# Kernel optimization log

Hardware: AMD Instinct MI355X
Metric: run time of the kernel (lower is better)

The kernel has to match this reference:

```python
import jax, jax.numpy as jnp
import numpy as np

BS, N, DIM, HEADS = 4, 2048, 512, 8
HEAD_DIM = DIM // HEADS
SCALE = HEAD_DIM ** 0.5
NEG = -1000000.0


def setup_inputs() -> dict:
    key = jax.random.key(0)
    ks = jax.random.split(key, 6)
    x = jax.random.normal(ks[0], (BS, N, DIM), dtype=jnp.float32)
    mask = jax.random.randint(ks[1], (BS, N), 0, 2, dtype=jnp.int32)
    s = 1.0 / np.sqrt(DIM)
    Wq = jax.random.normal(ks[2], (DIM, DIM), dtype=jnp.float32) * s
    Wk = jax.random.normal(ks[3], (DIM, DIM), dtype=jnp.float32) * s
    Wv = jax.random.normal(ks[4], (DIM, DIM), dtype=jnp.float32) * s
    Wo = jax.random.normal(ks[5], (DIM, DIM), dtype=jnp.float32) * s
    return {"x": x, "Wq": Wq, "Wk": Wk, "Wv": Wv, "Wo": Wo, "mask": mask}


def reference(x, Wq, Wk, Wv, Wo, mask):
    # q,k,v: (bs, n, dim) -> (bs, h, n, d)
    def split_heads(t):
        return t.reshape(BS, N, HEADS, HEAD_DIM).transpose(0, 2, 1, 3)
    q = split_heads(x @ Wq.T)
    k = split_heads(x @ Wk.T)
    v = split_heads(x @ Wv.T)
    # scores: (bs, h, n, n)
    scores = jnp.einsum('bhqd,bhkd->bhqk', q, k) / SCALE
    # key-padding mask broadcast over heads and query positions
    keep = (mask == 1)[:, None, None, :]  # (bs,1,1,n)
    scores = jnp.where(keep, scores, NEG)
    attn = jax.nn.softmax(scores, axis=-1)
    out = jnp.einsum('bhqk,bhkd->bhqd', attn, v)
    out = out.transpose(0, 2, 1, 3).reshape(BS, N, DIM)
    return out @ Wo.T
```

## Files before the change

### kernel.cpp

```cpp
#include <hip/hip_runtime.h>
#include <hip/hip_bf16.h>

#define BS 4
#define SEQ 2048
#define DIM 512
#define HEADS 8
#define HD 64
#define ROWS (BS*SEQ)
#define SCL2E 0.1803368801111244f
#define NEGB (-1.4426950408889634e6f)

typedef __attribute__((ext_vector_type(8))) short bf16x8;
typedef __attribute__((ext_vector_type(4))) short bf16x4;
typedef __attribute__((ext_vector_type(4))) float floatx4;
typedef unsigned short u16;
typedef unsigned int u32;

__device__ __forceinline__ u16 f2bf(float f) {
    union { float f; unsigned u; } v; v.f = f;
    unsigned r = v.u + 0x7fff + ((v.u >> 16) & 1);
    return (u16)(r >> 16);
}

__device__ __forceinline__ unsigned pack2bf(float a, float b) {
#if __has_builtin(__builtin_amdgcn_cvt_pk_bf16_f32)
    typedef __attribute__((ext_vector_type(2))) __bf16 bf2;
    union { bf2 v; unsigned u; } cv;
    cv.v = __builtin_amdgcn_cvt_pk_bf16_f32(a, b);
    return cv.u;
#else
    return (unsigned)f2bf(a) | ((unsigned)f2bf(b) << 16);
#endif
}

__device__ __forceinline__ float fexp2(float x) {
#if __has_builtin(__builtin_amdgcn_exp2f)
    return __builtin_amdgcn_exp2f(x);
#else
    return __expf(x * 0.6931471805599453f);
#endif
}

__device__ __forceinline__ void gload16(const u16* g, u16* l) {
    __builtin_amdgcn_global_load_lds(
        (const __attribute__((address_space(1))) u32*)g,
        (__attribute__((address_space(3))) u32*)l, 16, 0, 0);
}

__global__ __launch_bounds__(256) void convert_all(
    const float* __restrict__ x, const float* __restrict__ Wq,
    const float* __restrict__ Wk, const float* __restrict__ Wv,
    const float* __restrict__ Wo, const int* __restrict__ mask,
    u16* __restrict__ xb, u16* __restrict__ wqb,
    u16* __restrict__ wkb, u16* __restrict__ wvb,
    u16* __restrict__ wob, float* __restrict__ biasf)
{
    int i = blockIdx.x * 256 + threadIdx.x;
    if (i < 1048576 + 262144) {
        const float* src; u16* dst; int off;
        if (i < 1048576) { src = x; dst = xb; off = i; }
        else {
            int j = i - 1048576; int seg = j >> 16; off = j & 65535;
            src = seg == 0 ? Wq : seg == 1 ? Wk : seg == 2 ? Wv : Wo;
            dst = seg == 0 ? wqb : seg == 1 ? wkb : seg == 2 ? wvb : wob;
        }
        float4 v = ((const float4*)src)[off];
        ushort4 o;
        o.x = f2bf(v.x); o.y = f2bf(v.y); o.z = f2bf(v.z); o.w = f2bf(v.w);
        ((ushort4*)dst)[off] = o;
    } else {
        int jb = i - 1310720;
        int4 mv = ((const int4*)mask)[jb];
        float4 bo;
        bo.x = (mv.x == 1) ? 0.f : NEGB;
        bo.y = (mv.y == 1) ? 0.f : NEGB;
        bo.z = (mv.z == 1) ? 0.f : NEGB;
        bo.w = (mv.w == 1) ? 0.f : NEGB;
        ((float4*)biasf)[jb] = bo;
    }
}

__global__ __launch_bounds__(256, 3) void gemm_qkv_fused(
    const u16* __restrict__ A, const u16* __restrict__ Wcat,
    u16* __restrict__ Oq, u16* __restrict__ Okf, u16* __restrict__ Ovf)
{
    __shared__ u16 ldsA[8192];
    __shared__ u16 ldsB[8192];

    int n0 = blockIdx.x * 128;
    int m0 = blockIdx.y * 128;
    int tid = threadIdx.x;
    int w = tid >> 6, lane = tid & 63, quad = lane >> 4, l16 = lane & 15;
    int mo = (w & 1) * 64, no = (w >> 1) * 64;
    int l7 = l16 & 7;

    int sr = lane >> 3, sc = lane & 7, gc = sc ^ sr;
    const u16* gA0 = A    + (long)(m0 + sr) * DIM + gc * 8;
    const u16* gB0 = Wcat + (long)(n0 + sr) * DIM + gc * 8;

    floatx4 acc[4][4];
    #pragma unroll
    for (int mt = 0; mt < 4; mt++)
        #pragma unroll
        for (int nt = 0; nt < 4; nt++) acc[mt][nt] = (floatx4){0.f,0.f,0.f,0.f};

    for (int k0 = 0; k0 < DIM; k0 += 64) {
        #pragma unroll
        for (int i = 0; i < 4; i++) {
            int ch = w * 4 + i;
            gload16(gA0 + (long)ch * 8 * DIM + k0, &ldsA[ch * 512]);
            gload16(gB0 + (long)ch * 8 * DIM + k0, &ldsB[ch * 512]);
        }
        __syncthreads();

        #pragma unroll
        for (int kc = 0; kc < 2; kc++) {
            int swz = ((kc * 4 + quad) ^ l7) * 8;
            bf16x8 af[4], bf[4];
            #pragma unroll
            for (int t4 = 0; t4 < 4; t4++) {
                af[t4] = *(const bf16x8*)&ldsA[(mo + t4*16 + l16) * 64 + swz];
                bf[t4] = *(const bf16x8*)&ldsB[(no + t4*16 + l16) * 64 + swz];
            }
            #pragma unroll
            for (int mt = 0; mt < 4; mt++)
                #pragma unroll
                for (int nt = 0; nt < 4; nt++)
                    acc[mt][nt] = __builtin_amdgcn_mfma_f32_16x16x32_bf16(
                        af[mt], bf[nt], acc[mt][nt], 0, 0, 0);
        }
        __syncthreads();
    }

    int seg = n0 >> 9;
    if (seg == 0) {
        #pragma unroll
        for (int mt = 0; mt < 4; mt++)
            #pragma unroll
            for (int nt = 0; nt < 4; nt++)
                #pragma unroll
                for (int r = 0; r < 4; r++) {
                    int row = m0 + mo + mt*16 + quad*4 + r;
                    int col9 = (n0 + no + nt*16 + l16) & 511;
                    int b = row >> 11, n = row & 2047, h = col9 >> 6, d = col9 & 63;
                    Oq[(((long)(b * HEADS + h) * SEQ + n) << 6) + d] = f2bf(acc[mt][nt][r]);
                }
    } else if (seg == 1) {
        #pragma unroll
        for (int mt = 0; mt < 4; mt++)
            #pragma unroll
            for (int nt = 0; nt < 4; nt++)
                #pragma unroll
                for (int r = 0; r < 4; r++) {
                    int row = m0 + mo + mt*16 + quad*4 + r;
                    int col9 = (n0 + no + nt*16 + l16) & 511;
                    int b = row >> 11, keyn = row & 2047, h = col9 >> 6, dd = col9 & 63;
                    int kt = keyn >> 6, ntk = (keyn >> 4) & 3, l16k = keyn & 15;
                    int g = dd >> 5, quadk = (dd >> 3) & 3, j = dd & 7;
                    long offv = ((long)((b*HEADS + h)*32 + kt) << 12)
                              + ((ntk*2 + g) << 9) + ((quadk*16 + l16k) << 3) + j;
                    Okf[offv] = f2bf(acc[mt][nt][r] * SCL2E);
                }
    } else {
        #pragma unroll
        for (int mt = 0; mt < 4; mt++)
            #pragma unroll
            for (int nt = 0; nt < 4; nt++) {
                int rowb = m0 + mo + mt*16 + quad*4;
                int col9 = (n0 + no + nt*16 + l16) & 511;
                int b = rowb >> 11, keyn = rowb & 2047, h = col9 >> 6;
                int tile = (keyn >> 6) & 31;
                long offv = ((long)((b*HEADS + h)*32 + tile) << 12)
                          + ((long)(mt >> 1) << 11) + (nt << 9)
                          + ((quad*16 + l16) << 3) + ((mt & 1) << 2);
                ushort4 st;
                st.x = f2bf(acc[mt][nt][0]); st.y = f2bf(acc[mt][nt][1]);
                st.z = f2bf(acc[mt][nt][2]); st.w = f2bf(acc[mt][nt][3]);
                *(ushort4*)&Ovf[offv] = st;
            }
    }
}

__global__ __launch_bounds__(256, 3) void flash_attn(
    const u16* __restrict__ Q, const u16* __restrict__ Kf,
    const u16* __restrict__ Vf, const float* __restrict__ biasf,
    u16* __restrict__ ctx)
{
    __shared__ float red[4224];

    int bx = blockIdx.x;
    int cx = bx & 7, sx = bx >> 3;
    int gg = ((sx >> 5) << 3) | cx;
    int qi = sx & 31;
    int q0 = qi * 64;
    int h  = gg & 7;
    int b  = gg >> 3;
    int bh = b * HEADS + h;

    int tid = threadIdx.x;
    int w = tid >> 6, lane = tid & 63, quad = lane >> 4, l16 = lane & 15;
    int wq = w >> 1, wk = w & 1;

    bf16x8 qA0, qA1, qB0, qB1;
    {
        const u16* qp = Q + ((long)bh * SEQ + q0 + wq*32 + l16) * HD + quad * 8;
        qA0 = *(const bf16x8*)(qp);
        qA1 = *(const bf16x8*)(qp + 32);
        qB0 = *(const bf16x8*)(qp + 16*HD);
        qB1 = *(const bf16x8*)(qp + 16*HD + 32);
    }

    const u16* Kw = Kf + ((long)bh << 17) + wk*2048 + lane*8;
    const u16* Vw = Vf + ((long)bh << 17) + wk*2048 + lane*8;
    const float* bw = biasf + b * SEQ + wk*32 + quad*4;

    short one_s = (l16 == 0) ? (short)0x3F80 : (short)0;
    bf16x8 ones8 = { one_s, one_s, one_s, one_s, one_s, one_s, one_s, one_s };

    bf16x8 kA0 = *(const bf16x8*)(Kw);
    bf16x8 kA1 = *(const bf16x8*)(Kw + 512);
    bf16x8 kB0 = *(const bf16x8*)(Kw + 1024);
    bf16x8 kB1 = *(const bf16x8*)(Kw + 1536);
    bf16x8 vb0 = *(const bf16x8*)(Vw);
    bf16x8 vb1 = *(const bf16x8*)(Vw + 512);
    bf16x8 vb2 = *(const bf16x8*)(Vw + 1024);
    bf16x8 vb3 = *(const bf16x8*)(Vw + 1536);
    float4 bv0 = *(const float4*)(bw);
    float4 bv1 = *(const float4*)(bw + 16);

    floatx4 oA[4], oB[4], o5A, o5B;
    #pragma unroll
    for (int ct = 0; ct < 4; ct++) {
        oA[ct] = (floatx4){0.f,0.f,0.f,0.f};
        oB[ct] = (floatx4){0.f,0.f,0.f,0.f};
    }
    o5A = (floatx4){0.f,0.f,0.f,0.f};
    o5B = (floatx4){0.f,0.f,0.f,0.f};

    #pragma unroll 2
    for (int it = 0; it < 32; it++) {
        bf16x8 kA0n=kA0, kA1n=kA1, kB0n=kB0, kB1n=kB1;
        bf16x8 vb0n=vb0, vb1n=vb1, vb2n=vb2, vb3n=vb3;
        float4 bv0n=bv0, bv1n=bv1;
        if (it < 31) {
            const u16* kp = Kw + (long)(it+1)*4096;
            const u16* vp = Vw + (long)(it+1)*4096;
            kA0n = *(const bf16x8*)(kp);
            kA1n = *(const bf16x8*)(kp + 512);
            kB0n = *(const bf16x8*)(kp + 1024);
            kB1n = *(const bf16x8*)(kp + 1536);
            vb0n = *(const bf16x8*)(vp);
            vb1n = *(const bf16x8*)(vp + 512);
            vb2n = *(const bf16x8*)(vp + 1024);
            vb3n = *(const bf16x8*)(vp + 1536);
            bv0n = *(const float4*)(bw + (it+1)*64);
            bv1n = *(const float4*)(bw + (it+1)*64 + 16);
        }

        {
            floatx4 s0, s1;
            s0[0] = bv0.x; s0[1] = bv0.y; s0[2] = bv0.z; s0[3] = bv0.w;
            s1[0] = bv1.x; s1[1] = bv1.y; s1[2] = bv1.z; s1[3] = bv1.w;
            s0 = __builtin_amdgcn_mfma_f32_16x16x32_bf16(kA0, qA0, s0, 0, 0, 0);
            s0 = __builtin_amdgcn_mfma_f32_16x16x32_bf16(kA1, qA1, s0, 0, 0, 0);
            s1 = __builtin_amdgcn_mfma_f32_16x16x32_bf16(kB0, qA0, s1, 0, 0, 0);
            s1 = __builtin_amdgcn_mfma_f32_16x16x32_bf16(kB1, qA1, s1, 0, 0, 0);
            float p0 = fexp2(s0[0]);
            float p1 = fexp2(s0[1]);
            float p2 = fexp2(s0[2]);
            float p3 = fexp2(s0[3]);
            float p4 = fexp2(s1[0]);
            float p5 = fexp2(s1[1]);
            float p6 = fexp2(s1[2]);
            float p7 = fexp2(s1[3]);
            union { bf16x8 v; unsigned u[4]; } pu;
            pu.u[0] = pack2bf(p0, p1);
            pu.u[1] = pack2bf(p2, p3);
            pu.u[2] = pack2bf(p4, p5);
            pu.u[3] = pack2bf(p6, p7);
            oA[0] = __builtin_amdgcn_mfma_f32_16x16x32_bf16(pu.v, vb0, oA[0], 0, 0, 0);
            oA[1] = __builtin_amdgcn_mfma_f32_16x16x32_bf16(pu.v, vb1, oA[1], 0, 0, 0);
            oA[2] = __builtin_amdgcn_mfma_f32_16x16x32_bf16(pu.v, vb2, oA[2], 0, 0, 0);
            oA[3] = __builtin_amdgcn_mfma_f32_16x16x32_bf16(pu.v, vb3, oA[3], 0, 0, 0);
            o5A  = __builtin_amdgcn_mfma_f32_16x16x32_bf16(pu.v, ones8, o5A, 0, 0, 0);
        }
        {
            floatx4 s0, s1;
            s0[0] = bv0.x; s0[1] = bv0.y; s0[2] = bv0.z; s0[3] = bv0.w;
            s1[0] = bv1.x; s1[1] = bv1.y; s1[2] = bv1.z; s1[3] = bv1.w;
            s0 = __builtin_amdgcn_mfma_f32_16x16x32_bf16(kA0, qB0, s0, 0, 0, 0);
            s0 = __builtin_amdgcn_mfma_f32_16x16x32_bf16(kA1, qB1, s0, 0, 0, 0);
            s1 = __builtin_amdgcn_mfma_f32_16x16x32_bf16(kB0, qB0, s1, 0, 0, 0);
            s1 = __builtin_amdgcn_mfma_f32_16x16x32_bf16(kB1, qB1, s1, 0, 0, 0);
            float p0 = fexp2(s0[0]);
            float p1 = fexp2(s0[1]);
            float p2 = fexp2(s0[2]);
            float p3 = fexp2(s0[3]);
            float p4 = fexp2(s1[0]);
            float p5 = fexp2(s1[1]);
            float p6 = fexp2(s1[2]);
            float p7 = fexp2(s1[3]);
            union { bf16x8 v; unsigned u[4]; } pu;
            pu.u[0] = pack2bf(p0, p1);
            pu.u[1] = pack2bf(p2, p3);
            pu.u[2] = pack2bf(p4, p5);
            pu.u[3] = pack2bf(p6, p7);
            oB[0] = __builtin_amdgcn_mfma_f32_16x16x32_bf16(pu.v, vb0, oB[0], 0, 0, 0);
            oB[1] = __builtin_amdgcn_mfma_f32_16x16x32_bf16(pu.v, vb1, oB[1], 0, 0, 0);
            oB[2] = __builtin_amdgcn_mfma_f32_16x16x32_bf16(pu.v, vb2, oB[2], 0, 0, 0);
            oB[3] = __builtin_amdgcn_mfma_f32_16x16x32_bf16(pu.v, vb3, oB[3], 0, 0, 0);
            o5B  = __builtin_amdgcn_mfma_f32_16x16x32_bf16(pu.v, ones8, o5B, 0, 0, 0);
        }

        kA0 = kA0n; kA1 = kA1n; kB0 = kB0n; kB1 = kB1n;
        vb0 = vb0n; vb1 = vb1n; vb2 = vb2n; vb3 = vb3n;
        bv0 = bv0n; bv1 = bv1n;
    }

    floatx4* ldsv = (floatx4*)red;
    float* ldsf = red;
    int Town = wq*2 + wk;
    int Tpar = wq*2 + (wk ^ 1);

    if (wk == 0) {
        #pragma unroll
        for (int ct = 0; ct < 4; ct++)
            ldsv[Tpar*256 + ct*64 + lane] = oB[ct];
    } else {
        #pragma unroll
        for (int ct = 0; ct < 4; ct++)
            ldsv[Tpar*256 + ct*64 + lane] = oA[ct];
    }
    if (l16 == 0) {
        #pragma unroll
        for (int r = 0; r < 4; r++) {
            ldsf[4096 + ((wq*2 + 0)*2 + wk)*16 + quad*4 + r] = o5A[r];
            ldsf[4096 + ((wq*2 + 1)*2 + wk)*16 + quad*4 + r] = o5B[r];
        }
    }
    __syncthreads();

    float inv[4];
    #pragma unroll
    for (int r = 0; r < 4; r++) {
        float sden = ldsf[4096 + (Town*2 + 0)*16 + quad*4 + r]
                   + ldsf[4096 + (Town*2 + 1)*16 + quad*4 + r];
        inv[r] = 1.0f / sden;
    }

    #pragma unroll
    for (int ct = 0; ct < 4; ct++) {
        floatx4 part = ldsv[Town*256 + ct*64 + lane];
        floatx4 of = (wk == 0) ? oA[ct] : oB[ct];
        of += part;
        int col = h * HD + ct*16 + l16;
        long rb = (long)(b * SEQ + q0 + Town*16 + quad*4);
        #pragma unroll
        for (int r = 0; r < 4; r++)
            ctx[(rb + r) * DIM + col] = f2bf(of[r] * inv[r]);
    }
}

__global__ __launch_bounds__(256, 4) void gemm_proj(
    const u16* __restrict__ A, const u16* __restrict__ Bt,
    float* __restrict__ Out)
{
    __shared__ u16 ldsA[4096];
    __shared__ u16 ldsB[8192];

    int n0 = blockIdx.x * 128;
    int m0 = blockIdx.y * 64;
    int tid = threadIdx.x;
    int w = tid >> 6, lane = tid & 63, quad = lane >> 4, l16 = lane & 15;
    int l7 = l16 & 7;

    int sr = lane >> 3, sc = lane & 7, gc = sc ^ sr;
    const u16* gA0 = A  + (long)(m0 + sr) * DIM + gc * 8;
    const u16* gB0 = Bt + (long)(n0 + sr) * DIM + gc * 8;

    floatx4 acc[8];
    #pragma unroll
    for (int nt = 0; nt < 8; nt++) acc[nt] = (floatx4){0.f,0.f,0.f,0.f};

    for (int k0 = 0; k0 < DIM; k0 += 64) {
        gload16(gA0 + (long)(2*w)   * 8 * DIM + k0, &ldsA[(2*w)   * 512]);
        gload16(gA0 + (long)(2*w+1) * 8 * DIM + k0, &ldsA[(2*w+1) * 512]);
        #pragma unroll
        for (int i = 0; i < 4; i++)
            gload16(gB0 + (long)(4*w+i) * 8 * DIM + k0, &ldsB[(4*w+i) * 512]);
        __syncthreads();

        #pragma unroll
        for (int kc = 0; kc < 2; kc++) {
            int swz = ((kc * 4 + quad) ^ l7) * 8;
            bf16x8 af = *(const bf16x8*)&ldsA[(w*16 + l16) * 64 + swz];
            #pragma unroll
            for (int nt = 0; nt < 8; nt++) {
                bf16x8 bfv = *(const bf16x8*)&ldsB[(nt*16 + l16) * 64 + swz];
                acc[nt] = __builtin_amdgcn_mfma_f32_16x16x32_bf16(
                    af, bfv, acc[nt], 0, 0, 0);
            }
        }
        __syncthreads();
    }

    #pragma unroll
    for (int nt = 0; nt < 8; nt++)
        #pragma unroll
        for (int r = 0; r < 4; r++) {
            int row = m0 + w*16 + quad*4 + r;
            int col = n0 + nt*16 + l16;
            Out[(long)row * DIM + col] = acc[nt][r];
        }
}

extern "C" void kernel_launch(void* const* d_in, const int* in_sizes, int n_in,
                              void* d_out, int out_size, void* d_ws, size_t ws_size,
                              hipStream_t stream) {
    const float* x  = (const float*)d_in[0];
    const float* Wq = (const float*)d_in[1];
    const float* Wk = (const float*)d_in[2];
    const float* Wv = (const float*)d_in[3];
    const float* Wo = (const float*)d_in[4];
    const int* mask = (const int*)d_in[5];
    float* out = (float*)d_out;

    char* ws = (char*)d_ws;
    size_t off = 0;
    u16* xb  = (u16*)(ws + off); off += (size_t)ROWS * DIM * 2;
    u16* wqb = (u16*)(ws + off); off += (size_t)DIM * DIM * 2;
    u16* wkb = (u16*)(ws + off); off += (size_t)DIM * DIM * 2;
    u16* wvb = (u16*)(ws + off); off += (size_t)DIM * DIM * 2;
    u16* wob = (u16*)(ws + off); off += (size_t)DIM * DIM * 2;
    u16* Qh  = (u16*)(ws + off); off += (size_t)ROWS * DIM * 2;
    u16* Kfr = (u16*)(ws + off); off += (size_t)ROWS * DIM * 2;
    u16* Vfr = (u16*)(ws + off); off += (size_t)ROWS * DIM * 2;
    u16* ctx = (u16*)(ws + off); off += (size_t)ROWS * DIM * 2;
    float* biasf = (float*)(ws + off); off += (size_t)BS * SEQ * 4;

    convert_all<<<5128, 256, 0, stream>>>(x, Wq, Wk, Wv, Wo, mask,
                                          xb, wqb, wkb, wvb, wob, biasf);
    gemm_qkv_fused<<<dim3(12, 64), 256, 0, stream>>>(xb, wqb, Qh, Kfr, Vfr);
    flash_attn<<<BS * HEADS * (SEQ / 64), 256, 0, stream>>>(Qh, Kfr, Vfr, biasf, ctx);
    gemm_proj<<<dim3(4, 128), 256, 0, stream>>>(ctx, wob, out);

    (void)in_sizes; (void)n_in; (void)out_size; (void)ws_size;
}
```

Measured before the change: 165.3 us.

## Split keys across four waves with each wave covering all 64 queries

Restructures flash attention so each of the four waves handles a quarter of the keys for all 64 query rows, instead of a 2x2 split of queries and keys. Each K/V fragment is now reused across four query tiles, and each wave runs half as many loop iterations. The partial outputs are summed through shared memory in three sync rounds. It also wraps the MFMA groups in s_setprio. In exchange, register pressure rises from the larger accumulator array, occupancy is lowered to 2 waves, and the final cross-wave reduction is longer.

```diff
diff --git a/kernel.cpp b/kernel.cpp
--- a/kernel.cpp
+++ b/kernel.cpp
@@ -181,12 +181,12 @@
     }
 }
 
-__global__ __launch_bounds__(256, 3) void flash_attn(
+__global__ __launch_bounds__(256, 2) void flash_attn(
     const u16* __restrict__ Q, const u16* __restrict__ Kf,
     const u16* __restrict__ Vf, const float* __restrict__ biasf,
     u16* __restrict__ ctx)
 {
-    __shared__ float red[4224];
+    __shared__ float red[4352];
 
     int bx = blockIdx.x;
     int cx = bx & 7, sx = bx >> 3;
@@ -199,28 +199,26 @@
 
     int tid = threadIdx.x;
     int w = tid >> 6, lane = tid & 63, quad = lane >> 4, l16 = lane & 15;
-    int wq = w >> 1, wk = w & 1;
-
-    bf16x8 qA0, qA1, qB0, qB1;
-    {
-        const u16* qp = Q + ((long)bh * SEQ + q0 + wq*32 + l16) * HD + quad * 8;
-        qA0 = *(const bf16x8*)(qp);
-        qA1 = *(const bf16x8*)(qp + 32);
-        qB0 = *(const bf16x8*)(qp + 16*HD);
-        qB1 = *(const bf16x8*)(qp + 16*HD + 32);
-    }
-
-    const u16* Kw = Kf + ((long)bh << 17) + wk*2048 + lane*8;
-    const u16* Vw = Vf + ((long)bh << 17) + wk*2048 + lane*8;
-    const float* bw = biasf + b * SEQ + wk*32 + quad*4;
+
+    bf16x8 qb[4][2];
+    #pragma unroll
+    for (int nt = 0; nt < 4; nt++) {
+        const u16* qp = Q + ((long)bh * SEQ + q0 + nt*16 + l16) * HD + quad * 8;
+        qb[nt][0] = *(const bf16x8*)(qp);
+        qb[nt][1] = *(const bf16x8*)(qp + 32);
+    }
+
+    const u16* Kw = Kf + ((long)bh << 17) + w*2048 + lane*8;
+    const u16* Vw = Vf + ((long)bh << 17) + w*2048 + lane*8;
+    const float* bw = biasf + b * SEQ + w*32 + quad*4;
 
     short one_s = (l16 == 0) ? (short)0x3F80 : (short)0;
     bf16x8 ones8 = { one_s, one_s, one_s, one_s, one_s, one_s, one_s, one_s };
 
-    bf16x8 kA0 = *(const bf16x8*)(Kw);
-    bf16x8 kA1 = *(const bf16x8*)(Kw + 512);
-    bf16x8 kB0 = *(const bf16x8*)(Kw + 1024);
-    bf16x8 kB1 = *(const bf16x8*)(Kw + 1536);
+    bf16x8 k00 = *(const bf16x8*)(Kw);
+    bf16x8 k01 = *(const bf16x8*)(Kw + 512);
+    bf16x8 k10 = *(const bf16x8*)(Kw + 1024);
+    bf16x8 k11 = *(const bf16x8*)(Kw + 1536);
     bf16x8 vb0 = *(const bf16x8*)(Vw);
     bf16x8 vb1 = *(const bf16x8*)(Vw + 512);
     bf16x8 vb2 = *(const bf16x8*)(Vw + 1024);
@@ -228,43 +226,46 @@
     float4 bv0 = *(const float4*)(bw);
     float4 bv1 = *(const float4*)(bw + 16);
 
-    floatx4 oA[4], oB[4], o5A, o5B;
-    #pragma unroll
-    for (int ct = 0; ct < 4; ct++) {
-        oA[ct] = (floatx4){0.f,0.f,0.f,0.f};
-        oB[ct] = (floatx4){0.f,0.f,0.f,0.f};
-    }
-    o5A = (floatx4){0.f,0.f,0.f,0.f};
-    o5B = (floatx4){0.f,0.f,0.f,0.f};
+    floatx4 o[4][4];
+    floatx4 o5[4];
+    #pragma unroll
+    for (int nt = 0; nt < 4; nt++) {
+        #pragma unroll
+        for (int ct = 0; ct < 4; ct++) o[nt][ct] = (floatx4){0.f,0.f,0.f,0.f};
+        o5[nt] = (floatx4){0.f,0.f,0.f,0.f};
+    }
 
     #pragma unroll 2
-    for (int it = 0; it < 32; it++) {
-        bf16x8 kA0n=kA0, kA1n=kA1, kB0n=kB0, kB1n=kB1;
+    for (int it = 0; it < 16; it++) {
+        bf16x8 k00n=k00, k01n=k01, k10n=k10, k11n=k11;
         bf16x8 vb0n=vb0, vb1n=vb1, vb2n=vb2, vb3n=vb3;
         float4 bv0n=bv0, bv1n=bv1;
-        if (it < 31) {
-            const u16* kp = Kw + (long)(it+1)*4096;
-            const u16* vp = Vw + (long)(it+1)*4096;
-            kA0n = *(const bf16x8*)(kp);
-            kA1n = *(const bf16x8*)(kp + 512);
-            kB0n = *(const bf16x8*)(kp + 1024);
-            kB1n = *(const bf16x8*)(kp + 1536);
+        if (it < 15) {
+            const u16* kp = Kw + (long)(it+1)*8192;
+            const u16* vp = Vw + (long)(it+1)*8192;
+            k00n = *(const bf16x8*)(kp);
+            k01n = *(const bf16x8*)(kp + 512);
+            k10n = *(const bf16x8*)(kp + 1024);
+            k11n = *(const bf16x8*)(kp + 1536);
             vb0n = *(const bf16x8*)(vp);
             vb1n = *(const bf16x8*)(vp + 512);
             vb2n = *(const bf16x8*)(vp + 1024);
             vb3n = *(const bf16x8*)(vp + 1536);
-            bv0n = *(const float4*)(bw + (it+1)*64);
-            bv1n = *(const float4*)(bw + (it+1)*64 + 16);
-        }
-
-        {
+            bv0n = *(const float4*)(bw + (it+1)*128);
+            bv1n = *(const float4*)(bw + (it+1)*128 + 16);
+        }
+
+        #pragma unroll
+        for (int nt = 0; nt < 4; nt++) {
             floatx4 s0, s1;
             s0[0] = bv0.x; s0[1] = bv0.y; s0[2] = bv0.z; s0[3] = bv0.w;
             s1[0] = bv1.x; s1[1] = bv1.y; s1[2] = bv1.z; s1[3] = bv1.w;
-            s0 = __builtin_amdgcn_mfma_f32_16x16x32_bf16(kA0, qA0, s0, 0, 0, 0);
-            s0 = __builtin_amdgcn_mfma_f32_16x16x32_bf16(kA1, qA1, s0, 0, 0, 0);
-            s1 = __builtin_amdgcn_mfma_f32_16x16x32_bf16(kB0, qA0, s1, 0, 0, 0);
-            s1 = __builtin_amdgcn_mfma_f32_16x16x32_bf16(kB1, qA1, s1, 0, 0, 0);
+            __builtin_amdgcn_s_setprio(1);
+            s0 = __builtin_amdgcn_mfma_f32_16x16x32_bf16(k00, qb[nt][0], s0, 0, 0, 0);
+            s0 = __builtin_amdgcn_mfma_f32_16x16x32_bf16(k01, qb[nt][1], s0, 0, 0, 0);
+            s1 = __builtin_amdgcn_mfma_f32_16x16x32_bf16(k10, qb[nt][0], s1, 0, 0, 0);
+            s1 = __builtin_amdgcn_mfma_f32_16x16x32_bf16(k11, qb[nt][1], s1, 0, 0, 0);
+            __builtin_amdgcn_s_setprio(0);
             float p0 = fexp2(s0[0]);
             float p1 = fexp2(s0[1]);
             float p2 = fexp2(s0[2]);
@@ -278,86 +279,75 @@
             pu.u[1] = pack2bf(p2, p3);
             pu.u[2] = pack2bf(p4, p5);
             pu.u[3] = pack2bf(p6, p7);
-            oA[0] = __builtin_amdgcn_mfma_f32_16x16x32_bf16(pu.v, vb0, oA[0], 0, 0, 0);
-            oA[1] = __builtin_amdgcn_mfma_f32_16x16x32_bf16(pu.v, vb1, oA[1], 0, 0, 0);
-            oA[2] = __builtin_amdgcn_mfma_f32_16x16x32_bf16(pu.v, vb2, oA[2], 0, 0, 0);
-            oA[3] = __builtin_amdgcn_mfma_f32_16x16x32_bf16(pu.v, vb3, oA[3], 0, 0, 0);
-            o5A  = __builtin_amdgcn_mfma_f32_16x16x32_bf16(pu.v, ones8, o5A, 0, 0, 0);
-        }
-        {
-            floatx4 s0, s1;
-            s0[0] = bv0.x; s0[1] = bv0.y; s0[2] = bv0.z; s0[3] = bv0.w;
-            s1[0] = bv1.x; s1[1] = bv1.y; s1[2] = bv1.z; s1[3] = bv1.w;
-            s0 = __builtin_amdgcn_mfma_f32_16x16x32_bf16(kA0, qB0, s0, 0, 0, 0);
-            s0 = __builtin_amdgcn_mfma_f32_16x16x32_bf16(kA1, qB1, s0, 0, 0, 0);
-            s1 = __builtin_amdgcn_mfma_f32_16x16x32_bf16(kB0, qB0, s1, 0, 0, 0);
-            s1 = __builtin_amdgcn_mfma_f32_16x16x32_bf16(kB1, qB1, s1, 0, 0, 0);
-            float p0 = fexp2(s0[0]);
-            float p1 = fexp2(s0[1]);
-            float p2 = fexp2(s0[2]);
-            float p3 = fexp2(s0[3]);
-            float p4 = fexp2(s1[0]);
-            float p5 = fexp2(s1[1]);
-            float p6 = fexp2(s1[2]);
-            float p7 = fexp2(s1[3]);
-            union { bf16x8 v; unsigned u[4]; } pu;
-            pu.u[0] = pack2bf(p0, p1);
-            pu.u[1] = pack2bf(p2, p3);
-            pu.u[2] = pack2bf(p4, p5);
-            pu.u[3] = pack2bf(p6, p7);
-            oB[0] = __builtin_amdgcn_mfma_f32_16x16x32_bf16(pu.v, vb0, oB[0], 0, 0, 0);
-            oB[1] = __builtin_amdgcn_mfma_f32_16x16x32_bf16(pu.v, vb1, oB[1], 0, 0, 0);
-            oB[2] = __builtin_amdgcn_mfma_f32_16x16x32_bf16(pu.v, vb2, oB[2], 0, 0, 0);
-            oB[3] = __builtin_amdgcn_mfma_f32_16x16x32_bf16(pu.v, vb3, oB[3], 0, 0, 0);
-            o5B  = __builtin_amdgcn_mfma_f32_16x16x32_bf16(pu.v, ones8, o5B, 0, 0, 0);
-        }
-
-        kA0 = kA0n; kA1 = kA1n; kB0 = kB0n; kB1 = kB1n;
+            __builtin_amdgcn_s_setprio(1);
+            o[nt][0] = __builtin_amdgcn_mfma_f32_16x16x32_bf16(pu.v, vb0, o[nt][0], 0, 0, 0);
+            o[nt][1] = __builtin_amdgcn_mfma_f32_16x16x32_bf16(pu.v, vb1, o[nt][1], 0, 0, 0);
+            o[nt][2] = __builtin_amdgcn_mfma_f32_16x16x32_bf16(pu.v, vb2, o[nt][2], 0, 0, 0);
+            o[nt][3] = __builtin_amdgcn_mfma_f32_16x16x32_bf16(pu.v, vb3, o[nt][3], 0, 0, 0);
+            o5[nt] = __builtin_amdgcn_mfma_f32_16x16x32_bf16(pu.v, ones8, o5[nt], 0, 0, 0);
+            __builtin_amdgcn_s_setprio(0);
+        }
+
+        k00 = k00n; k01 = k01n; k10 = k10n; k11 = k11n;
         vb0 = vb0n; vb1 = vb1n; vb2 = vb2n; vb3 = vb3n;
         bv0 = bv0n; bv1 = bv1n;
     }
 
+    __syncthreads();
+    float* ldsf = red;
     floatx4* ldsv = (floatx4*)red;
-    float* ldsf = red;
-    int Town = wq*2 + wk;
-    int Tpar = wq*2 + (wk ^ 1);
-
-    if (wk == 0) {
-        #pragma unroll
-        for (int ct = 0; ct < 4; ct++)
-            ldsv[Tpar*256 + ct*64 + lane] = oB[ct];
-    } else {
-        #pragma unroll
-        for (int ct = 0; ct < 4; ct++)
-            ldsv[Tpar*256 + ct*64 + lane] = oA[ct];
-    }
+
     if (l16 == 0) {
         #pragma unroll
+        for (int nt = 0; nt < 4; nt++)
+            #pragma unroll
+            for (int r = 0; r < 4; r++)
+                ldsf[4096 + w*64 + nt*16 + quad*4 + r] = o5[nt][r];
+    }
+    __syncthreads();
+
+    #pragma unroll
+    for (int i2 = 1; i2 < 4; i2++) {
+        int tslot = (w + i2) & 3;
+        #pragma unroll
+        for (int nt = 0; nt < 4; nt++)
+            if (nt == tslot) {
+                #pragma unroll
+                for (int ct = 0; ct < 4; ct++)
+                    ldsv[nt*256 + ct*64 + lane] = o[nt][ct];
+            }
+        __syncthreads();
+        #pragma unroll
+        for (int nt = 0; nt < 4; nt++)
+            if (nt == w) {
+                #pragma unroll
+                for (int ct = 0; ct < 4; ct++) {
+                    floatx4 v = ldsv[nt*256 + ct*64 + lane];
+                    o[nt][ct] += v;
+                }
+            }
+        __syncthreads();
+    }
+
+    #pragma unroll
+    for (int nt = 0; nt < 4; nt++) {
+        if (nt != w) continue;
+        float inv[4];
+        #pragma unroll
         for (int r = 0; r < 4; r++) {
-            ldsf[4096 + ((wq*2 + 0)*2 + wk)*16 + quad*4 + r] = o5A[r];
-            ldsf[4096 + ((wq*2 + 1)*2 + wk)*16 + quad*4 + r] = o5B[r];
-        }
-    }
-    __syncthreads();
-
-    float inv[4];
-    #pragma unroll
-    for (int r = 0; r < 4; r++) {
-        float sden = ldsf[4096 + (Town*2 + 0)*16 + quad*4 + r]
-                   + ldsf[4096 + (Town*2 + 1)*16 + quad*4 + r];
-        inv[r] = 1.0f / sden;
-    }
-
-    #pragma unroll
-    for (int ct = 0; ct < 4; ct++) {
-        floatx4 part = ldsv[Town*256 + ct*64 + lane];
-        floatx4 of = (wk == 0) ? oA[ct] : oB[ct];
-        of += part;
-        int col = h * HD + ct*16 + l16;
-        long rb = (long)(b * SEQ + q0 + Town*16 + quad*4);
-        #pragma unroll
-        for (int r = 0; r < 4; r++)
-            ctx[(rb + r) * DIM + col] = f2bf(of[r] * inv[r]);
+            int q = w*16 + quad*4 + r;
+            float sden = ldsf[4096 + q] + ldsf[4096 + 64 + q]
+                       + ldsf[4096 + 128 + q] + ldsf[4096 + 192 + q];
+            inv[r] = 1.0f / sden;
+        }
+        #pragma unroll
+        for (int ct = 0; ct < 4; ct++) {
+            int col = h * HD + ct*16 + l16;
+            long rb = (long)(b * SEQ + q0 + w*16 + quad*4);
+            #pragma unroll
+            for (int r = 0; r < 4; r++)
+                ctx[(rb + r) * DIM + col] = f2bf(o[nt][ct][r] * inv[r]);
+        }
     }
 }
 
```

After: 161.0 us. 2.6% less time.
